# Performance work log

Measured on AMD Instinct MI355X. Metric: run time of the kernel, lower is better.

The kernel has to match this reference:

```python
import jax, jax.numpy as jnp
import numpy as np


def setup_inputs() -> dict:
    key = jax.random.key(0)
    k1, k2, k3, k4 = jax.random.split(key, 4)
    batch, T, state_dim, action_dim = 64, 1024, 512, 128
    x0 = jax.random.normal(k1, (batch, state_dim), dtype=jnp.float32)
    us = jax.random.normal(k2, (batch, T, action_dim), dtype=jnp.float32)
    # Scale A so the 1024-step linear recurrence stays bounded (spectral radius < 1)
    A = jax.random.normal(k3, (state_dim, state_dim), dtype=jnp.float32) * (0.9 / np.sqrt(state_dim))
    B = jax.random.normal(k4, (action_dim, state_dim), dtype=jnp.float32) * (1.0 / np.sqrt(action_dim))
    return {"x0": x0, "us": us, "A": A, "B": B}


def reference(x0, us, A, B):
    """Linear SSM rollout: x_{t+1} = x_t @ A + u_t @ B, returns xs [batch, T, state_dim]."""
    us_t = jnp.swapaxes(us, 0, 1)  # [T, batch, action_dim]

    def step(x, u):
        x_next = x @ A + u @ B  # [batch, state_dim]
        return x_next, x_next

    _, xs = jax.lax.scan(step, x0, us_t)  # xs: [T, batch, state_dim]
    return jnp.swapaxes(xs, 0, 1)  # [batch, T, state_dim]
```

## Files before the change

### kernel.cpp

```cpp
#include <hip/hip_runtime.h>


typedef __attribute__((ext_vector_type(8))) short bf16x8;
typedef __attribute__((ext_vector_type(8))) unsigned short ushort8;
typedef __attribute__((ext_vector_type(4))) float f32x4;
typedef unsigned short ushort_t;

#define MFMA16(a, b, c) __builtin_amdgcn_mfma_f32_16x16x32_bf16(a, b, c, 0, 0, 0)

#define OFF_AT  0UL
#define OFF_AU  8912896UL
#define OFF_BT  15204352UL
#define OFF_BU  15335424UL
#define OFF_WT  15466496UL
#define OFF_Z   16515072UL
#define OFF_E1S 41680896UL
#define OFF_E2S 50069504UL

__host__ __device__ __forceinline__ int slot_of(int p) {
    if (p == 0) return 16;
    if (p <= 8) return p - 1;
    return 7 + (p >> 3);
}

__device__ __forceinline__ unsigned short f2bf(float f) {
    union { float f; unsigned u; } v; v.f = f;
    unsigned r = v.u + 0x7FFFu + ((v.u >> 16) & 1u);
    return (unsigned short)(r >> 16);
}

__device__ __forceinline__ int sel4(int4 v, int p) {
    return p == 0 ? v.x : p == 1 ? v.y : p == 2 ? v.z : v.w;
}

typedef __attribute__((address_space(3))) unsigned int as3_u32;
typedef __attribute__((address_space(1))) const unsigned int as1_u32;
__device__ __forceinline__ void gll16(const void* g, void* l) {
    __builtin_amdgcn_global_load_lds((as1_u32*)g, (as3_u32*)l, 16, 0, 0);
}

__global__ __launch_bounds__(256) void prep_kernel(const float* __restrict__ A,
                                                   char* __restrict__ ws) {
    ushort_t* At1 = (ushort_t*)(ws + OFF_AT);
    ushort_t* Au1 = (ushort_t*)(ws + OFF_AU);
    long idx = (long)blockIdx.x * 256 + threadIdx.x;
    if (idx < 262144) {
        Au1[idx] = f2bf(A[idx]);
    } else {
        long gi = idx - 262144;
        int n = (int)(gi >> 9), k = (int)(gi & 511);
        At1[gi] = f2bf(A[(long)k * 512 + n]);
    }
}

__device__ __forceinline__ void pow_tile(char* __restrict__ ws, ushort_t* ldsX,
                                         int d, int m_, int i_, int prod,
                                         int mb, int nb) {
    ushort_t* At = (ushort_t*)(ws + OFF_AT);
    ushort_t* Au = (ushort_t*)(ws + OFF_AU);
    const ushort_t *Xp, *Yp; ushort_t* outp;
    if (prod == 0) { Xp = At + (long)slot_of(m_) * 262144; Yp = Au + (long)slot_of(i_) * 262144; outp = At + (long)slot_of(d) * 262144; }
    else           { Xp = Au + (long)slot_of(i_) * 262144; Yp = At + (long)slot_of(m_) * 262144; outp = Au + (long)slot_of(d) * 262144; }

    int tid = threadIdx.x, w = tid >> 6, lane = tid & 63, q = lane >> 4, r = lane & 15;

    for (int i2 = tid; i2 < 64 * 64; i2 += 256) {
        int row = i2 >> 6, c8 = i2 & 63;
        ushort8 v = *(const ushort8*)(Xp + (long)(mb * 64 + row) * 512 + c8 * 8);
        *(ushort8*)&ldsX[row * 512 + ((c8 ^ (row & 7)) << 3)] = v;
    }
    __syncthreads();

    f32x4 acc[4][2];
    for (int a1 = 0; a1 < 4; a1++) for (int b1 = 0; b1 < 2; b1++) acc[a1][b1] = (f32x4){0.f, 0.f, 0.f, 0.f};

    int n0 = nb * 128 + w * 32;
    for (int kt = 0; kt < 16; kt++) {
        bf16x8 b0 = *(const bf16x8*)(Yp + (long)(n0 + r) * 512 + kt * 32 + q * 8);
        bf16x8 b1 = *(const bf16x8*)(Yp + (long)(n0 + 16 + r) * 512 + kt * 32 + q * 8);
        int g2 = kt * 4 + q;
#pragma unroll
        for (int mi = 0; mi < 4; mi++) {
            int row = mi * 16 + r;
            bf16x8 a = *(bf16x8*)&ldsX[row * 512 + ((g2 ^ (row & 7)) << 3)];
            acc[mi][0] = MFMA16(a, b0, acc[mi][0]);
            acc[mi][1] = MFMA16(a, b1, acc[mi][1]);
        }
    }
    for (int mi = 0; mi < 4; mi++) for (int nj = 0; nj < 2; nj++) {
        int m = mb * 64 + mi * 16 + q * 4, n = n0 + nj * 16 + r;
        for (int v = 0; v < 4; v++) outp[(long)(m + v) * 512 + n] = f2bf(acc[mi][nj][v]);
    }
}

__device__ __forceinline__ void wk_tile(char* __restrict__ ws, ushort_t* ldsX,
                                        int k8, int mb) {
    ushort_t* At = (ushort_t*)(ws + OFF_AT);
    ushort_t* Bu = (ushort_t*)(ws + OFF_BU);
    ushort_t* Bt = (ushort_t*)(ws + OFF_BT);
    ushort_t* Wt = (ushort_t*)(ws + OFF_WT);

    int tid = threadIdx.x, w = tid >> 6, lane = tid & 63, q = lane >> 4, r = lane & 15;

    if (k8 == 7) {
        for (int i2 = tid; i2 < 64 * 32; i2 += 256) {
            int row = i2 >> 5, c4 = i2 & 31;
            ushort4 v = *(const ushort4*)(Bt + (long)(mb * 64 + row) * 128 + c4 * 4);
            *(ushort4*)(Wt + (long)(mb * 64 + row) * 128 + c4 * 4) = v;
        }
        return;
    }

    int p = 7 - k8;
    const ushort_t* Xp = At + (long)slot_of(p) * 262144;
    for (int i2 = tid; i2 < 64 * 64; i2 += 256) {
        int row = i2 >> 6, c8 = i2 & 63;
        ushort8 v = *(const ushort8*)(Xp + (long)(mb * 64 + row) * 512 + c8 * 8);
        *(ushort8*)&ldsX[row * 512 + ((c8 ^ (row & 7)) << 3)] = v;
    }
    __syncthreads();

    f32x4 acc[4][2];
    for (int a1 = 0; a1 < 4; a1++) for (int b1 = 0; b1 < 2; b1++) acc[a1][b1] = (f32x4){0.f, 0.f, 0.f, 0.f};

    int n0 = w * 32;
    for (int kt = 0; kt < 16; kt++) {
        bf16x8 b0 = *(const bf16x8*)(Bu + (long)(n0 + r) * 512 + kt * 32 + q * 8);
        bf16x8 b1 = *(const bf16x8*)(Bu + (long)(n0 + 16 + r) * 512 + kt * 32 + q * 8);
        int g2 = kt * 4 + q;
#pragma unroll
        for (int mi = 0; mi < 4; mi++) {
            int row = mi * 16 + r;
            bf16x8 a = *(bf16x8*)&ldsX[row * 512 + ((g2 ^ (row & 7)) << 3)];
            acc[mi][0] = MFMA16(a, b0, acc[mi][0]);
            acc[mi][1] = MFMA16(a, b1, acc[mi][1]);
        }
    }
    ushort_t* Wp = Wt + (long)p * 65536;
    for (int mi = 0; mi < 4; mi++) for (int nj = 0; nj < 2; nj++) {
        int m = mb * 64 + mi * 16 + q * 4, n = n0 + nj * 16 + r;
        for (int v = 0; v < 4; v++) Wp[(long)(m + v) * 128 + n] = f2bf(acc[mi][nj][v]);
    }
}

__global__ __launch_bounds__(256) void pow_stage(char* __restrict__ ws,
                                                 const float* __restrict__ us,
                                                 const float* __restrict__ x0,
                                                 const float* __restrict__ B,
                                                 int4 dd, int4 mm, int4 ii,
                                                 int dual, int wkbase,
                                                 int ubase, int umode,
                                                 int ustart, int uend) {
    __shared__ ushort_t ldsX[64 * 512];
    int bx = blockIdx.x;

    if (ubase > 0 && bx >= ubase) {
        int tid = threadIdx.x;
        int nthr = (256 - ubase) * 256;
        if (umode == 0) {
            ushort_t* Z = (ushort_t*)(ws + OFF_Z);
            for (long gi = ustart + (long)(bx - ubase) * 256 + tid; gi < uend; gi += nthr) {
                int row = (int)(gi >> 7), g8 = (int)(gi & 127);
                int c = row >> 6, b = row & 63;
                const float* src = us + (long)b * 131072 + c * 1024 + g8 * 8;
                float4 v0 = *(const float4*)src;
                float4 v1 = *(const float4*)(src + 4);
                ushort8 h = { f2bf(v0.x), f2bf(v0.y), f2bf(v0.z), f2bf(v0.w),
                              f2bf(v1.x), f2bf(v1.y), f2bf(v1.z), f2bf(v1.w) };
                *(ushort8*)(Z + (long)row * 1536 + 512 + g8 * 8) = h;
            }
        } else {
            ushort_t* Bt  = (ushort_t*)(ws + OFF_BT);
            ushort_t* Bu  = (ushort_t*)(ws + OFF_BU);
            ushort_t* X0b = (ushort_t*)(ws + OFF_E2S);
            ushort_t* At1 = (ushort_t*)(ws + OFF_AT);
            for (long i = (long)(bx - ubase) * 256 + tid; i < 331776; i += nthr) {
                if (i < 65536) {
                    int kp = (int)(i >> 9), n = (int)(i & 511);
                    ushort_t v = f2bf(B[i]);
                    Bt[(long)n * 128 + kp] = v;
                    Bu[i] = v;
                } else if (i < 69632) {
                    long gi = i - 65536;
                    long e0 = gi * 8;
                    float4 v0 = *(const float4*)(x0 + e0);
                    float4 v1 = *(const float4*)(x0 + e0 + 4);
                    ushort8 h = { f2bf(v0.x), f2bf(v0.y), f2bf(v0.z), f2bf(v0.w),
                                  f2bf(v1.x), f2bf(v1.y), f2bf(v1.z), f2bf(v1.w) };
                    *(ushort8*)(X0b + e0) = h;
                } else {
                    long gi2 = i - 69632;
                    int n = (int)(gi2 >> 9), k2 = (int)(gi2 & 511);
                    At1[(long)16 * 262144 + gi2] = (n == k2) ? (ushort_t)0x3F80 : (ushort_t)0;
                }
            }
        }
        return;
    }
    if (wkbase > 0 && bx >= wkbase) {
        int widx = bx - wkbase;
        wk_tile(ws, ldsX, widx >> 3, widx & 7);
        return;
    }

    int nb = bx & 3, mb = (bx >> 2) & 7;
    int prod, pair;
    if (dual) { prod = (bx >> 5) & 1; pair = bx >> 6; }
    else      { prod = 0;             pair = bx >> 5; }
    int d = sel4(dd, pair), m_ = sel4(mm, pair), i_ = sel4(ii, pair);
    pow_tile(ws, ldsX, d, m_, i_, prod, mb, nb);
}

__global__ __launch_bounds__(256, 4) void e1g(char* __restrict__ ws) {
    __shared__ ushort_t Alds[64 * 64];
    __shared__ ushort_t Blds[128 * 64];
    const ushort_t* Z  = (const ushort_t*)(ws + OFF_Z);
    const ushort_t* Wt = (const ushort_t*)(ws + OFF_WT);
    ushort_t* E1s = (ushort_t*)(ws + OFF_E1S);

    int bx = blockIdx.x;
    int c = bx >> 2, nt = bx & 3;
    int tid = threadIdx.x, w = tid >> 6, lane = tid & 63, q = lane >> 4, r = lane & 15;
    int wr = w >> 1, wc = w & 1;
    int l8 = lane >> 3, srcg = (lane & 7) ^ l8;

    const ushort_t* Xb = Z + (long)c * 64 * 1536 + 512;

    f32x4 acc[2][4];
#pragma unroll
    for (int a1 = 0; a1 < 2; a1++)
#pragma unroll
        for (int b1 = 0; b1 < 4; b1++) acc[a1][b1] = (f32x4){0.f, 0.f, 0.f, 0.f};

    for (int s = 0; s < 16; s++) {
        int k0 = s * 64;
#pragma unroll
        for (int i = 0; i < 2; i++) {
            int row = i * 32 + w * 8 + l8;
            gll16(Xb + (long)row * 1536 + k0 + srcg * 8, &Alds[i * 2048 + w * 512]);
        }
        const ushort_t* Yb = Wt + (long)(7 - (s >> 1)) * 65536 + (s & 1) * 64;
#pragma unroll
        for (int i = 0; i < 4; i++) {
            int row = i * 32 + w * 8 + l8;
            gll16(Yb + (long)(nt * 128 + row) * 128 + srcg * 8, &Blds[i * 2048 + w * 512]);
        }
        __syncthreads();
#pragma unroll
        for (int kt = 0; kt < 2; kt++) {
            int g2 = kt * 4 + q;
            bf16x8 a[2], b[4];
#pragma unroll
            for (int mi = 0; mi < 2; mi++) {
                int row = wr * 32 + mi * 16 + r;
                a[mi] = *(bf16x8*)&Alds[row * 64 + ((g2 ^ (row & 7)) << 3)];
            }
#pragma unroll
            for (int nj = 0; nj < 4; nj++) {
                int row = wc * 64 + nj * 16 + r;
                b[nj] = *(bf16x8*)&Blds[row * 64 + ((g2 ^ (row & 7)) << 3)];
            }
#pragma unroll
            for (int mi = 0; mi < 2; mi++)
#pragma unroll
                for (int nj = 0; nj < 4; nj++)
                    acc[mi][nj] = MFMA16(a[mi], b[nj], acc[mi][nj]);
        }
        __syncthreads();
    }

#pragma unroll
    for (int mi = 0; mi < 2; mi++)
#pragma unroll
        for (int nj = 0; nj < 4; nj++) {
            int m = wr * 32 + mi * 16 + q * 4;
            int n = nt * 128 + wc * 64 + nj * 16 + r;
#pragma unroll
            for (int v = 0; v < 4; v++)
                E1s[(long)c * 32768 + (long)(m + v) * 512 + n] = f2bf(acc[mi][nj][v]);
        }
}

__global__ __launch_bounds__(256, 4) void e2g(char* __restrict__ ws) {
    __shared__ ushort_t Alds[32 * 64];
    __shared__ ushort_t Blds[32 * 64];
    const ushort_t* At  = (const ushort_t*)(ws + OFF_AT);
    const ushort_t* E1s = (const ushort_t*)(ws + OFF_E1S);
    ushort_t* E2s = (ushort_t*)(ws + OFF_E2S);

    int bx = blockIdx.x;
    int g = bx >> 5, mb = (bx >> 4) & 1, ntb = bx & 15;
    int tid = threadIdx.x, w = tid >> 6, lane = tid & 63, q = lane >> 4, r = lane & 15;
    int wr = w >> 1, wc = w & 1;
    int l8 = lane >> 3, srcg = (lane & 7) ^ l8;

    f32x4 acc = (f32x4){0.f, 0.f, 0.f, 0.f};

    for (int s = 0; s < 64; s++) {
        int t = s >> 3, k0 = (s & 7) * 64;
        const ushort_t* Xp = E1s + (long)(8 * g + t) * 32768 + (long)mb * 32 * 512;
        const ushort_t* Yb = At + (long)slot_of(8 * (7 - t)) * 262144;
        {
            int row = w * 8 + l8;
            gll16(Xp + (long)row * 512 + k0 + srcg * 8, &Alds[w * 512]);
            gll16(Yb + (long)(ntb * 32 + row) * 512 + k0 + srcg * 8, &Blds[w * 512]);
        }
        __syncthreads();
#pragma unroll
        for (int kt = 0; kt < 2; kt++) {
            int g2 = kt * 4 + q;
            int arow = wr * 16 + r;
            bf16x8 a = *(bf16x8*)&Alds[arow * 64 + ((g2 ^ (arow & 7)) << 3)];
            int brow = wc * 16 + r;
            bf16x8 b = *(bf16x8*)&Blds[brow * 64 + ((g2 ^ (brow & 7)) << 3)];
            acc = MFMA16(a, b, acc);
        }
        __syncthreads();
    }

    {
        int m = mb * 32 + wr * 16 + q * 4;
        int n = ntb * 32 + wc * 16 + r;
#pragma unroll
        for (int v = 0; v < 4; v++)
            E2s[(long)(1 + g) * 32768 + (long)(m + v) * 512 + n] = f2bf(acc[v]);
    }
}

__global__ __launch_bounds__(256, 4) void s1x(float* __restrict__ dout,
                                              char* __restrict__ ws) {
    __shared__ ushort_t Alds[64 * 64];
    __shared__ ushort_t Blds[128 * 64];
    const ushort_t* At  = (const ushort_t*)(ws + OFF_AT);
    const ushort_t* E1s = (const ushort_t*)(ws + OFF_E1S);
    const ushort_t* E2s = (const ushort_t*)(ws + OFF_E2S);
    ushort_t* Z = (ushort_t*)(ws + OFF_Z);

    int bx = blockIdx.x;
    int t0 = bx >> 2, nt = bx & 3;
    int g, j;
    if (t0 == 128) { g = 16; j = 0; }
    else {
        g = t0 >> 3;
        int jj = t0 & 7;
        j = (g >= 8) ? (7 - jj) : jj;
    }
    int c = g * 8 + j;
    int extra = (j == 0 && g >= 1) ? 1 : 0;
    int nterms = 1 + extra + j;
    int S = nterms * 8;
    int tid = threadIdx.x, w = tid >> 6, lane = tid & 63, q = lane >> 4, r = lane & 15;
    int wr = w >> 1, wc = w & 1;
    int l8 = lane >> 3, srcg = (lane & 7) ^ l8;

    auto xptr = [&](int t) -> const ushort_t* {
        if (t == 0) return E2s + (long)g * 32768;
        if (extra && t == 1) return E2s + (long)(g - 1) * 32768;
        return E1s + (long)(8 * g + t - 1 - extra) * 32768;
    };
    auto yptr = [&](int t) -> const ushort_t* {
        int p = (t == 0) ? 8 * j : ((extra && t == 1) ? 64 : 8 * (j - t + extra));
        return At + (long)slot_of(p) * 262144;
    };

    f32x4 acc[2][4];
#pragma unroll
    for (int a1 = 0; a1 < 2; a1++)
#pragma unroll
        for (int b1 = 0; b1 < 4; b1++) acc[a1][b1] = (f32x4){0.f, 0.f, 0.f, 0.f};

    for (int s = 0; s < S; s++) {
        int t = s >> 3, k0 = (s & 7) * 64;
        const ushort_t* Xp = xptr(t);
        const ushort_t* Yb = yptr(t);
#pragma unroll
        for (int i = 0; i < 2; i++) {
            int row = i * 32 + w * 8 + l8;
            gll16(Xp + (long)row * 512 + k0 + srcg * 8, &Alds[i * 2048 + w * 512]);
        }
#pragma unroll
        for (int i = 0; i < 4; i++) {
            int row = i * 32 + w * 8 + l8;
            gll16(Yb + (long)(nt * 128 + row) * 512 + k0 + srcg * 8, &Blds[i * 2048 + w * 512]);
        }
        __syncthreads();
#pragma unroll
        for (int kt = 0; kt < 2; kt++) {
            int g2 = kt * 4 + q;
            bf16x8 a[2], b[4];
#pragma unroll
            for (int mi = 0; mi < 2; mi++) {
                int row = wr * 32 + mi * 16 + r;
                a[mi] = *(bf16x8*)&Alds[row * 64 + ((g2 ^ (row & 7)) << 3)];
            }
#pragma unroll
            for (int nj = 0; nj < 4; nj++) {
                int row = wc * 64 + nj * 16 + r;
                b[nj] = *(bf16x8*)&Blds[row * 64 + ((g2 ^ (row & 7)) << 3)];
            }
#pragma unroll
            for (int mi = 0; mi < 2; mi++)
#pragma unroll
                for (int nj = 0; nj < 4; nj++)
                    acc[mi][nj] = MFMA16(a[mi], b[nj], acc[mi][nj]);
        }
        __syncthreads();
    }

#pragma unroll
    for (int mi = 0; mi < 2; mi++)
#pragma unroll
        for (int nj = 0; nj < 4; nj++) {
            int m = wr * 32 + mi * 16 + q * 4;
            int n = nt * 128 + wc * 64 + nj * 16 + r;
#pragma unroll
            for (int v = 0; v < 4; v++) {
                float val = acc[mi][nj][v];
                int row = m + v;
                if (c < 128)
                    Z[(long)(c * 64 + row) * 1536 + n] = f2bf(val);
                if (c >= 1)
                    dout[(long)row * 524288 + (long)(8 * c - 1) * 512 + n] = val;
            }
        }
}

__global__ __launch_bounds__(256, 4) void outg(float* __restrict__ dout,
                                               char* __restrict__ ws) {
    __shared__ ushort_t Alds[128 * 64];
    __shared__ ushort_t Blds[128 * 64];
    const ushort_t* Z  = (const ushort_t*)(ws + OFF_Z);
    const ushort_t* At = (const ushort_t*)(ws + OFF_AT);
    const ushort_t* Wt = (const ushort_t*)(ws + OFF_WT);

    int bx = blockIdx.x;
    int nt = bx / 448;
    int rem = bx - nt * 448;
    int k = 6 - (rem >> 6);
    int mt = rem & 63;
    int tid = threadIdx.x, w = tid >> 6, lane = tid & 63, q = lane >> 4, r = lane & 15;
    int wr = w >> 1, wc = w & 1;
    int l8 = lane >> 3, srcg = (lane & 7) ^ l8;

    const ushort_t* Xb = Z + (long)mt * 128 * 1536;
    const ushort_t* Ya = At + (long)slot_of(k + 1) * 262144;
    int Ks = 8 + 2 * (k + 1);

    f32x4 acc[4][4];
#pragma unroll
    for (int a1 = 0; a1 < 4; a1++)
#pragma unroll
        for (int b1 = 0; b1 < 4; b1++) acc[a1][b1] = (f32x4){0.f, 0.f, 0.f, 0.f};

    for (int s = 0; s < Ks; s++) {
        int k0 = s * 64;
#pragma unroll
        for (int i = 0; i < 4; i++) {
            int row = i * 32 + w * 8 + l8;
            gll16(Xb + (long)row * 1536 + k0 + srcg * 8, &Alds[i * 2048 + w * 512]);
        }
        if (k0 < 512) {
#pragma unroll
            for (int i = 0; i < 4; i++) {
                int row = i * 32 + w * 8 + l8;
                gll16(Ya + (long)(nt * 128 + row) * 512 + k0 + srcg * 8, &Blds[i * 2048 + w * 512]);
            }
        } else {
            int uc = k0 - 512;
            const ushort_t* Yb = Wt + (long)(k - (uc >> 7)) * 65536 + (uc & 127);
#pragma unroll
            for (int i = 0; i < 4; i++) {
                int row = i * 32 + w * 8 + l8;
                gll16(Yb + (long)(nt * 128 + row) * 128 + srcg * 8, &Blds[i * 2048 + w * 512]);
            }
        }
        __syncthreads();
#pragma unroll
        for (int kt = 0; kt < 2; kt++) {
            int g2 = kt * 4 + q;
            bf16x8 a[4], b[4];
#pragma unroll
            for (int mi = 0; mi < 4; mi++) {
                int row = wr * 64 + mi * 16 + r;
                a[mi] = *(bf16x8*)&Alds[row * 64 + ((g2 ^ (row & 7)) << 3)];
            }
#pragma unroll
            for (int nj = 0; nj < 4; nj++) {
                int row = wc * 64 + nj * 16 + r;
                b[nj] = *(bf16x8*)&Blds[row * 64 + ((g2 ^ (row & 7)) << 3)];
            }
#pragma unroll
            for (int mi = 0; mi < 4; mi++)
#pragma unroll
                for (int nj = 0; nj < 4; nj++)
                    acc[mi][nj] = MFMA16(a[mi], b[nj], acc[mi][nj]);
        }
        __syncthreads();
    }

#pragma unroll
    for (int mi = 0; mi < 4; mi++) {
        int m = mt * 128 + wr * 64 + mi * 16 + q * 4;
#pragma unroll
        for (int nj = 0; nj < 4; nj++) {
            int n = nt * 128 + wc * 64 + nj * 16 + r;
#pragma unroll
            for (int v = 0; v < 4; v++) {
                int mm = m + v;
                dout[(long)(mm & 63) * 524288 + (long)(((mm >> 6) << 3) + k) * 512 + n] = acc[mi][nj][v];
            }
        }
    }
}

extern "C" void kernel_launch(void* const* d_in, const int* in_sizes, int n_in,
                              void* d_out, int out_size, void* d_ws, size_t ws_size,
                              hipStream_t stream) {
    const float* x0 = (const float*)d_in[0];
    const float* us = (const float*)d_in[1];
    const float* A  = (const float*)d_in[2];
    const float* B  = (const float*)d_in[3];
    float* dout = (float*)d_out;
    char* ws = (char*)d_ws;

    prep_kernel<<<2048, 256, 0, stream>>>(A, ws);

    const int stdual[6]  = {1, 1, 1, 1, 1, 0};
    const int stwk[6]    = {0, 0, 0, 64, 0, 0};
    const int stub[6]    = {64, 128, 0, 128, 128, 128};
    const int stum[6]    = {1, 0, 0, 0, 0, 0};
    const int stus[6]    = {0, 0, 0, 262144, 524288, 786432};
    const int stue[6]    = {0, 262144, 0, 524288, 786432, 1048576};
    const int stpw[6]    = {64, 128, 256, 64, 128, 128};
    const int std_[6][4] = {{2,0,0,0},{3,4,0,0},{5,6,7,8},{16,0,0,0},{24,32,0,0},{40,48,56,64}};
    const int stm[6][4]  = {{1,0,0,0},{2,2,0,0},{4,4,4,4},{8,0,0,0},{16,16,0,0},{32,32,32,32}};
    const int sti[6][4]  = {{1,0,0,0},{1,2,0,0},{1,2,3,4},{8,0,0,0},{8,16,0,0},{8,16,24,32}};
    for (int s = 0; s < 6; s++) {
        int4 dd = {std_[s][0], std_[s][1], std_[s][2], std_[s][3]};
        int4 mm = {stm[s][0], stm[s][1], stm[s][2], stm[s][3]};
        int4 ii = {sti[s][0], sti[s][1], sti[s][2], sti[s][3]};
        int blocks = (stub[s] > 0) ? 256 : stpw[s] + stwk[s];
        pow_stage<<<blocks, 256, 0, stream>>>(ws, us, x0, B, dd, mm, ii,
                                              stdual[s], stwk[s], stub[s],
                                              stum[s], stus[s], stue[s]);
    }

    e1g<<<512, 256, 0, stream>>>(ws);
    e2g<<<512, 256, 0, stream>>>(ws);
    s1x<<<516, 256, 0, stream>>>(dout, ws);
    outg<<<1792, 256, 0, stream>>>(dout, ws);
}
```

Before: 246.8 us.

## Split output GEMM into two stages reusing the intermediate state at offset four

The final output kernel previously computed offsets 1..7 within each chunk directly from chunk-start states, using up to 24 K-steps for far offsets. Now outg handles offsets 0..3 and stores the offset-3 state as bf16 in a scratch buffer. A new outg2 kernel then computes offsets 4..6 from that state with shorter reductions. This reduces the total K-length of the GEMMs but adds a dependent launch and an extra bf16 rounding step on the intermediate state.

```diff
diff --git a/kernel.cpp b/kernel.cpp
--- a/kernel.cpp
+++ b/kernel.cpp
@@ -432,11 +432,12 @@
     const ushort_t* Z  = (const ushort_t*)(ws + OFF_Z);
     const ushort_t* At = (const ushort_t*)(ws + OFF_AT);
     const ushort_t* Wt = (const ushort_t*)(ws + OFF_WT);
+    ushort_t* M = (ushort_t*)(ws + OFF_E1S);
 
     int bx = blockIdx.x;
-    int nt = bx / 448;
-    int rem = bx - nt * 448;
-    int k = 6 - (rem >> 6);
+    int nt = bx >> 8;
+    int rem = bx & 255;
+    int k = 3 - (rem >> 6);
     int mt = rem & 63;
     int tid = threadIdx.x, w = tid >> 6, lane = tid & 63, q = lane >> 4, r = lane & 15;
     int wr = w >> 1, wc = w & 1;
@@ -507,7 +508,105 @@
 #pragma unroll
             for (int v = 0; v < 4; v++) {
                 int mm = m + v;
-                dout[(long)(mm & 63) * 524288 + (long)(((mm >> 6) << 3) + k) * 512 + n] = acc[mi][nj][v];
+                float val = acc[mi][nj][v];
+                dout[(long)(mm & 63) * 524288 + (long)(((mm >> 6) << 3) + k) * 512 + n] = val;
+                if (k == 3)
+                    M[(long)mm * 512 + n] = f2bf(val);
+            }
+        }
+    }
+}
+
+__global__ __launch_bounds__(256, 4) void outg2(float* __restrict__ dout,
+                                                char* __restrict__ ws) {
+    __shared__ ushort_t Alds[128 * 64];
+    __shared__ ushort_t Blds[128 * 64];
+    const ushort_t* Z  = (const ushort_t*)(ws + OFF_Z);
+    const ushort_t* At = (const ushort_t*)(ws + OFF_AT);
+    const ushort_t* Wt = (const ushort_t*)(ws + OFF_WT);
+    const ushort_t* M  = (const ushort_t*)(ws + OFF_E1S);
+
+    int bx = blockIdx.x;
+    int nt = bx / 192;
+    int rem = bx - nt * 192;
+    int kp = 2 - (rem >> 6);
+    int mt = rem & 63;
+    int tid = threadIdx.x, w = tid >> 6, lane = tid & 63, q = lane >> 4, r = lane & 15;
+    int wr = w >> 1, wc = w & 1;
+    int l8 = lane >> 3, srcg = (lane & 7) ^ l8;
+
+    const ushort_t* Xm = M + (long)mt * 128 * 512;
+    const ushort_t* Xu = Z + (long)mt * 128 * 1536 + 1024;
+    const ushort_t* Ya = At + (long)slot_of(kp + 1) * 262144;
+    int Ks = 8 + 2 * (kp + 1);
+
+    f32x4 acc[4][4];
+#pragma unroll
+    for (int a1 = 0; a1 < 4; a1++)
+#pragma unroll
+        for (int b1 = 0; b1 < 4; b1++) acc[a1][b1] = (f32x4){0.f, 0.f, 0.f, 0.f};
+
+    for (int s = 0; s < Ks; s++) {
+        int k0 = s * 64;
+        if (k0 < 512) {
+#pragma unroll
+            for (int i = 0; i < 4; i++) {
+                int row = i * 32 + w * 8 + l8;
+                gll16(Xm + (long)row * 512 + k0 + srcg * 8, &Alds[i * 2048 + w * 512]);
+            }
+#pragma unroll
+            for (int i = 0; i < 4; i++) {
+                int row = i * 32 + w * 8 + l8;
+                gll16(Ya + (long)(nt * 128 + row) * 512 + k0 + srcg * 8, &Blds[i * 2048 + w * 512]);
+            }
+        } else {
+            int uc = k0 - 512;
+#pragma unroll
+            for (int i = 0; i < 4; i++) {
+                int row = i * 32 + w * 8 + l8;
+                gll16(Xu + (long)row * 1536 + uc + srcg * 8, &Alds[i * 2048 + w * 512]);
+            }
+            const ushort_t* Yb = Wt + (long)(kp - (uc >> 7)) * 65536 + (uc & 127);
+#pragma unroll
+            for (int i = 0; i < 4; i++) {
+                int row = i * 32 + w * 8 + l8;
+                gll16(Yb + (long)(nt * 128 + row) * 128 + srcg * 8, &Blds[i * 2048 + w * 512]);
+            }
+        }
+        __syncthreads();
+#pragma unroll
+        for (int kt = 0; kt < 2; kt++) {
+            int g2 = kt * 4 + q;
+            bf16x8 a[4], b[4];
+#pragma unroll
+            for (int mi = 0; mi < 4; mi++) {
+                int row = wr * 64 + mi * 16 + r;
+                a[mi] = *(bf16x8*)&Alds[row * 64 + ((g2 ^ (row & 7)) << 3)];
+            }
+#pragma unroll
+            for (int nj = 0; nj < 4; nj++) {
+                int row = wc * 64 + nj * 16 + r;
+                b[nj] = *(bf16x8*)&Blds[row * 64 + ((g2 ^ (row & 7)) << 3)];
+            }
+#pragma unroll
+            for (int mi = 0; mi < 4; mi++)
+#pragma unroll
+                for (int nj = 0; nj < 4; nj++)
+                    acc[mi][nj] = MFMA16(a[mi], b[nj], acc[mi][nj]);
+        }
+        __syncthreads();
+    }
+
+#pragma unroll
+    for (int mi = 0; mi < 4; mi++) {
+        int m = mt * 128 + wr * 64 + mi * 16 + q * 4;
+#pragma unroll
+        for (int nj = 0; nj < 4; nj++) {
+            int n = nt * 128 + wc * 64 + nj * 16 + r;
+#pragma unroll
+            for (int v = 0; v < 4; v++) {
+                int mm = m + v;
+                dout[(long)(mm & 63) * 524288 + (long)(((mm >> 6) << 3) + 4 + kp) * 512 + n] = acc[mi][nj][v];
             }
         }
     }
@@ -548,5 +647,6 @@
     e1g<<<512, 256, 0, stream>>>(ws);
     e2g<<<512, 256, 0, stream>>>(ws);
     s1x<<<516, 256, 0, stream>>>(dout, ws);
-    outg<<<1792, 256, 0, stream>>>(dout, ws);
-}
+    outg<<<1024, 256, 0, stream>>>(dout, ws);
+    outg2<<<768, 256, 0, stream>>>(dout, ws);
+}
```

New measurement: 243.5 us (median of 2 runs). Within noise of the previous version (-1.3%).
